# Kernel optimization log

Measured on AMD Instinct MI355X. Metric: run time of the kernel, lower is better.

## Reference

```python
import math
import jax, jax.numpy as jnp
import numpy as np

DIM = 2048
N_HEADS = 16
HEAD_DIM = DIM // N_HEADS
HID = 5632  # multiple_of*ceil(int(2*(4*dim)/3)/multiple_of)
EPS = 1e-5
B, S = 2, 2048


def setup_inputs() -> dict:
    key = jax.random.key(0)
    ks = jax.random.split(key, 12)
    sd = 0.02
    return {
        "x": jax.random.normal(ks[0], (B, S, DIM), jnp.float32),
        "mask": jnp.zeros((1, 1, S, S), jnp.float32),
        "attn_bias": jax.random.normal(ks[1], (1, N_HEADS, S, S), jnp.float32) * 0.1,
        "wq": jax.random.normal(ks[2], (DIM, DIM), jnp.float32) * sd,
        "wk": jax.random.normal(ks[3], (DIM, DIM), jnp.float32) * sd,
        "wv": jax.random.normal(ks[4], (DIM, DIM), jnp.float32) * sd,
        "wo": jax.random.normal(ks[5], (DIM, DIM), jnp.float32) * sd,
        "w1": jax.random.normal(ks[6], (HID, DIM), jnp.float32) * sd,
        "w2": jax.random.normal(ks[7], (DIM, HID), jnp.float32) * sd,
        "w3": jax.random.normal(ks[8], (HID, DIM), jnp.float32) * sd,
        "attn_norm_w": jnp.ones((DIM,), jnp.float32),
        "ffn_norm_w": jnp.ones((DIM,), jnp.float32),
    }


def rmsnorm(x, w):
    x32 = x.astype(jnp.float32)
    y = x32 * jax.lax.rsqrt(jnp.mean(x32 * x32, axis=-1, keepdims=True) + EPS)
    return y.astype(x.dtype) * w


def reference(x, mask, attn_bias, wq, wk, wv, wo, w1, w2, w3, attn_norm_w, ffn_norm_w):
    b, s, _ = x.shape
    # --- attention ---
    h = rmsnorm(x, attn_norm_w)
    q = (h @ wq.T).reshape(b, s, N_HEADS, HEAD_DIM)
    k = (h @ wk.T).reshape(b, s, N_HEADS, HEAD_DIM)
    v = (h @ wv.T).reshape(b, s, N_HEADS, HEAD_DIM)
    scores = jnp.einsum("bqhd,bkhd->bhqk", q, k) / math.sqrt(HEAD_DIM)
    scores = scores + attn_bias + mask
    probs = jax.nn.softmax(scores.astype(jnp.float32), axis=-1).astype(q.dtype)
    out = jnp.einsum("bhqk,bkhd->bqhd", probs, v).reshape(b, s, DIM)
    h1 = x + out @ wo.T
    # --- SwiGLU FFN ---
    f = rmsnorm(h1, ffn_norm_w)
    ff = (jax.nn.silu(f @ w1.T) * (f @ w3.T)) @ w2.T
    return h1 + ff
```

## Files before the change

### kernel.cpp

```cpp
#include <hip/hip_runtime.h>
#include <stdint.h>

typedef uint16_t u16;
typedef __attribute__((ext_vector_type(8))) short s16x8;
typedef __attribute__((ext_vector_type(4))) float f32x4;

typedef const __attribute__((address_space(1))) void* gptr_t;
typedef __attribute__((address_space(3))) void* lptr_t;

__device__ __forceinline__ float bf2f(u16 u) { return __uint_as_float(((unsigned)u) << 16); }
__device__ __forceinline__ u16 f2bf(float f) {
    unsigned u = __float_as_uint(f);
    u += 0x7fffu + ((u >> 16) & 1u);
    return (u16)(u >> 16);
}
__device__ __forceinline__ void gld_lds16(const void* g, void* l) {
    __builtin_amdgcn_global_load_lds((gptr_t)g, (lptr_t)l, 16, 0, 0);
}

__global__ __launch_bounds__(256) void cvt_f32_bf16(const float* __restrict__ src,
                                                    u16* __restrict__ dst, long n)
{
    const long i = ((long)blockIdx.x * 256 + threadIdx.x) * 8;
    if (i >= n) return;
    float4 a = *(const float4*)(src + i);
    float4 b = *(const float4*)(src + i + 4);
    u16 o8[8] = { f2bf(a.x), f2bf(a.y), f2bf(a.z), f2bf(a.w),
                  f2bf(b.x), f2bf(b.y), f2bf(b.z), f2bf(b.w) };
    *(uint4*)(dst + i) = *(const uint4*)o8;
}

__global__ __launch_bounds__(512, 2) void gemm256(
        const u16* __restrict__ A, const u16* __restrict__ B,
        u16* __restrict__ Cb, int M, int N, int K, int gx)
{
    __shared__ __align__(16) u16 As[2][256 * 64];
    __shared__ __align__(16) u16 Bs[2][256 * 64];

    const int tid  = threadIdx.x;
    const int wave = tid >> 6, lane = tid & 63;
    const int quad = lane >> 4, l16 = lane & 15;
    const int wmi = wave >> 2, wni = wave & 3;

    const int cpx = gridDim.x >> 3;
    const int wg  = ((int)blockIdx.x & 7) * cpx + ((int)blockIdx.x >> 3);
    const long m0 = (long)(wg / gx) * 256;
    const long n0 = (long)(wg % gx) * 256;

    f32x4 acc[8][4] = {};

    const u16* Ag = A + m0 * (long)K;
    const u16* Bg = B + n0 * (long)K;
    long soff[4];
    int  lbase[4];
#pragma unroll
    for (int i = 0; i < 4; i++) {
        const int c = i * 512 + tid;
        const int row = c >> 3, col8 = (c & 7) * 8;
        soff[i]  = (long)row * K + (col8 ^ ((row & 7) << 3));
        lbase[i] = (i * 512 + wave * 64) * 8;
    }

#pragma unroll
    for (int i = 0; i < 4; i++) {
        gld_lds16(Ag + soff[i], &As[0][lbase[i]]);
        gld_lds16(Bg + soff[i], &Bs[0][lbase[i]]);
    }
    __syncthreads();

    const int swz   = (l16 & 7) << 3;
    const int arow0 = wmi * 128 + l16;
    const int brow0 = wni * 64 + l16;

    int db = 0;
    for (int k0 = 0; k0 < K; k0 += 64) {
        const int  kn = k0 + 64;
        const bool pf = kn < K;
        s16x8 bfrag[4][2];
#pragma unroll
        for (int p = 0; p < 4; p++) {
            if (pf) {
                gld_lds16(Ag + soff[p] + kn, &As[db ^ 1][lbase[p]]);
                gld_lds16(Bg + soff[p] + kn, &Bs[db ^ 1][lbase[p]]);
            }
            if (p == 0) {
#pragma unroll
                for (int nt = 0; nt < 4; nt++)
#pragma unroll
                    for (int kk = 0; kk < 2; kk++)
                        bfrag[nt][kk] = *(const s16x8*)&Bs[db][(brow0 + nt * 16) * 64
                                            + ((kk * 32 + quad * 8) ^ swz)];
            }
            s16x8 af[2][2];
#pragma unroll
            for (int mtl = 0; mtl < 2; mtl++)
#pragma unroll
                for (int kk = 0; kk < 2; kk++)
                    af[mtl][kk] = *(const s16x8*)&As[db][(arow0 + (2 * p + mtl) * 16) * 64
                                        + ((kk * 32 + quad * 8) ^ swz)];
            __builtin_amdgcn_s_setprio(1);
#pragma unroll
            for (int mtl = 0; mtl < 2; mtl++)
#pragma unroll
                for (int nt = 0; nt < 4; nt++)
#pragma unroll
                    for (int kk = 0; kk < 2; kk++)
                        acc[2 * p + mtl][nt] = __builtin_amdgcn_mfma_f32_16x16x32_bf16(
                            af[mtl][kk], bfrag[nt][kk], acc[2 * p + mtl][nt], 0, 0, 0);
            __builtin_amdgcn_s_setprio(0);
        }
        __syncthreads();
        db ^= 1;
    }

#pragma unroll
    for (int mt = 0; mt < 8; mt++)
#pragma unroll
        for (int nt = 0; nt < 4; nt++) {
            const long col = n0 + wni * 64 + nt * 16 + l16;
#pragma unroll
            for (int r = 0; r < 4; r++) {
                const long row = m0 + wmi * 128 + mt * 16 + quad * 4 + r;
                Cb[row * (long)N + col] = f2bf(acc[mt][nt][r]);
            }
        }
}

__global__ __launch_bounds__(256) void gemm_bt(
        const u16* __restrict__ A, const u16* __restrict__ B,
        u16* __restrict__ Cb, float* __restrict__ Cf, const float* __restrict__ Rf,
        int M, int N, int K, int lda, int ep)
{
    __shared__ __align__(16) u16 As[128 * 32];
    __shared__ __align__(16) u16 Bs[128 * 32];

    const int tid  = threadIdx.x;
    const int wave = tid >> 6, lane = tid & 63;
    const int quad = lane >> 4, l16 = lane & 15;
    const long m0 = (long)blockIdx.y * 128, n0 = (long)blockIdx.x * 128;
    const int wm = (wave >> 1) * 64, wn = (wave & 1) * 64;

    f32x4 acc[4][4] = {};

    const int c0 = tid, c1 = tid + 256;
    const u16* Ag = A + m0 * (long)lda;
    const u16* Bg = B + n0 * (long)K;
    const long aA0 = (long)(c0 >> 2) * lda + (c0 & 3) * 8;
    const long aA1 = (long)(c1 >> 2) * lda + (c1 & 3) * 8;
    const long aB0 = (long)(c0 >> 2) * K + (c0 & 3) * 8;
    const long aB1 = (long)(c1 >> 2) * K + (c1 & 3) * 8;
    const int lb0 = (wave * 64) * 8;
    const int lb1 = (256 + wave * 64) * 8;

    for (int k0 = 0; k0 < K; k0 += 32) {
        __syncthreads();
        gld_lds16(Ag + aA0 + k0, &As[lb0]);
        gld_lds16(Ag + aA1 + k0, &As[lb1]);
        gld_lds16(Bg + aB0 + k0, &Bs[lb0]);
        gld_lds16(Bg + aB1 + k0, &Bs[lb1]);
        __syncthreads();

        s16x8 af[4], bfr[4];
#pragma unroll
        for (int t = 0; t < 4; t++) {
            af[t]  = *(const s16x8*)&As[(wm + t * 16 + l16) * 32 + quad * 8];
            bfr[t] = *(const s16x8*)&Bs[(wn + t * 16 + l16) * 32 + quad * 8];
        }
#pragma unroll
        for (int mt = 0; mt < 4; mt++)
#pragma unroll
            for (int nt = 0; nt < 4; nt++)
                acc[mt][nt] = __builtin_amdgcn_mfma_f32_16x16x32_bf16(
                    af[mt], bfr[nt], acc[mt][nt], 0, 0, 0);
    }

#pragma unroll
    for (int mt = 0; mt < 4; mt++)
#pragma unroll
        for (int nt = 0; nt < 4; nt++) {
            const long col = n0 + wn + nt * 16 + l16;
#pragma unroll
            for (int r = 0; r < 4; r++) {
                const long row = m0 + wm + mt * 16 + quad * 4 + r;
                const long idx = row * N + col;
                const float v = acc[mt][nt][r];
                if (ep == 0) Cb[idx] = f2bf(v);
                else         Cf[idx] = v + Rf[idx];
            }
        }
}

__global__ __launch_bounds__(256) void flash_attn(
        const u16* __restrict__ Q, const u16* __restrict__ Kp,
        const u16* __restrict__ V, int ld, const float* __restrict__ bias,
        const float* __restrict__ mask, u16* __restrict__ O)
{
    const int tid  = threadIdx.x;
    const int wave = tid >> 6, lane = tid & 63;
    const int quad = lane >> 4, l16 = lane & 15;
    const int q0 = blockIdx.x * 64, h = blockIdx.y, b = blockIdx.z;

    __shared__ __align__(16) u16 Ks[64 * 128];
    __shared__ __align__(16) u16 Vt[128 * 64];
    __shared__ __align__(16) u16 Ps[4][16 * 64];

    const long baseI = (long)b * 2048 * ld + (long)h * 128;
    const long baseO = (long)b * 2048 * 2048 + (long)h * 128;

    s16x8 qf[4];
    {
        const u16* qp = Q + baseI + (long)(q0 + wave * 16 + l16) * ld;
#pragma unroll
        for (int kk = 0; kk < 4; kk++)
            qf[kk] = *(const s16x8*)(qp + kk * 32 + quad * 8);
    }

    f32x4 oacc[8] = {};
    float m_i[4] = { -1e30f, -1e30f, -1e30f, -1e30f };
    float l_i[4] = { 0.f, 0.f, 0.f, 0.f };
    const float scale = 0.08838834764831845f;
    const int kswz = (l16 & 7) << 3;

    for (int k0 = 0; k0 < 2048; k0 += 64) {
        __syncthreads();
#pragma unroll
        for (int it = 0; it < 4; it++) {
            const int c = it * 256 + tid;
            const int row = c >> 4, col8 = (c & 15) * 8;
            const int src = col8 ^ ((row & 7) << 3);
            gld_lds16(Kp + baseI + (long)(k0 + row) * ld + src,
                      &Ks[(it * 256 + wave * 64) * 8]);
        }
#pragma unroll
        for (int it = 0; it < 4; it++) {
            const int c = it * 256 + tid;
            const int row = c >> 4, col8 = (c & 15) * 8;
            uint4 raw = *(const uint4*)(V + baseI + (long)(k0 + row) * ld + col8);
            const u16* e = (const u16*)&raw;
#pragma unroll
            for (int j = 0; j < 8; j++) {
                const int d = col8 + j;
                const int swzv = ((d & 7) ^ ((d >> 3) & 7)) << 3;
                Vt[d * 64 + (row ^ swzv)] = e[j];
            }
        }
        __syncthreads();

        float sv[4][4];
#pragma unroll
        for (int nt = 0; nt < 4; nt++) {
            f32x4 sa = { 0.f, 0.f, 0.f, 0.f };
#pragma unroll
            for (int kk = 0; kk < 4; kk++) {
                s16x8 kf = *(const s16x8*)&Ks[(nt * 16 + l16) * 128
                                              + ((kk * 32 + quad * 8) ^ kswz)];
                sa = __builtin_amdgcn_mfma_f32_16x16x32_bf16(qf[kk], kf, sa, 0, 0, 0);
            }
            const int kcol = k0 + nt * 16 + l16;
#pragma unroll
            for (int r = 0; r < 4; r++) {
                const int qrow = q0 + wave * 16 + quad * 4 + r;
                float val = sa[r] * scale;
                val += bias[((long)h * 2048 + qrow) * 2048 + kcol];
                val += mask[(long)qrow * 2048 + kcol];
                sv[nt][r] = val;
            }
        }

        float alpha[4];
#pragma unroll
        for (int r = 0; r < 4; r++) {
            float mx = fmaxf(fmaxf(sv[0][r], sv[1][r]), fmaxf(sv[2][r], sv[3][r]));
#pragma unroll
            for (int off = 1; off < 16; off <<= 1) mx = fmaxf(mx, __shfl_xor(mx, off));
            const float mnew = fmaxf(m_i[r], mx);
            alpha[r] = __expf(m_i[r] - mnew);
            m_i[r] = mnew;
            float rs = 0.f;
#pragma unroll
            for (int nt = 0; nt < 4; nt++) {
                const float pv = __expf(sv[nt][r] - mnew);
                sv[nt][r] = pv;
                rs += pv;
            }
#pragma unroll
            for (int off = 1; off < 16; off <<= 1) rs += __shfl_xor(rs, off);
            l_i[r] = l_i[r] * alpha[r] + rs;
        }

#pragma unroll
        for (int nt = 0; nt < 4; nt++)
#pragma unroll
            for (int r = 0; r < 4; r++) {
                const int prow = quad * 4 + r;
                Ps[wave][prow * 64 + ((nt * 16 + l16) ^ ((prow & 7) << 3))]
                    = f2bf(sv[nt][r]);
            }

#pragma unroll
        for (int dt = 0; dt < 8; dt++)
#pragma unroll
            for (int r = 0; r < 4; r++)
                oacc[dt][r] *= alpha[r];

#pragma unroll
        for (int kk2 = 0; kk2 < 2; kk2++) {
            s16x8 pf = *(const s16x8*)&Ps[wave][l16 * 64
                                               + ((kk2 * 32 + quad * 8) ^ kswz)];
#pragma unroll
            for (int dt = 0; dt < 8; dt++) {
                const int d = dt * 16 + l16;
                const int vswz = ((d & 7) ^ ((d >> 3) & 7)) << 3;
                s16x8 vf = *(const s16x8*)&Vt[d * 64
                                              + ((kk2 * 32 + quad * 8) ^ vswz)];
                oacc[dt] = __builtin_amdgcn_mfma_f32_16x16x32_bf16(pf, vf, oacc[dt], 0, 0, 0);
            }
        }
    }

#pragma unroll
    for (int dt = 0; dt < 8; dt++)
#pragma unroll
        for (int r = 0; r < 4; r++) {
            const int qrow = q0 + wave * 16 + quad * 4 + r;
            O[baseO + (long)qrow * 2048 + dt * 16 + l16] = f2bf(oacc[dt][r] / l_i[r]);
        }
}

__global__ __launch_bounds__(256) void rmsnorm_f32(
        const float* __restrict__ x, const float* __restrict__ w,
        u16* __restrict__ out)
{
    const int row = blockIdx.x, tid = threadIdx.x;
    const float* xr = x + (long)row * 2048;
    float4 f0 = *(const float4*)(xr + tid * 8);
    float4 f1 = *(const float4*)(xr + tid * 8 + 4);
    float v[8] = { f0.x, f0.y, f0.z, f0.w, f1.x, f1.y, f1.z, f1.w };
    float ss = 0.f;
#pragma unroll
    for (int j = 0; j < 8; j++) ss += v[j] * v[j];
#pragma unroll
    for (int off = 32; off > 0; off >>= 1) ss += __shfl_xor(ss, off);
    __shared__ float red[4];
    if ((tid & 63) == 0) red[tid >> 6] = ss;
    __syncthreads();
    const float tot = red[0] + red[1] + red[2] + red[3];
    const float sc = rsqrtf(tot * (1.0f / 2048.0f) + 1e-5f);
    float4 w0 = *(const float4*)(w + tid * 8);
    float4 w1v = *(const float4*)(w + tid * 8 + 4);
    const float wv[8] = { w0.x, w0.y, w0.z, w0.w, w1v.x, w1v.y, w1v.z, w1v.w };
    u16 o8[8];
#pragma unroll
    for (int j = 0; j < 8; j++) o8[j] = f2bf(v[j] * sc * wv[j]);
    *(uint4*)(out + (long)row * 2048 + tid * 8) = *(const uint4*)o8;
}

__global__ __launch_bounds__(704) void silu_mul_rows(u16* __restrict__ s13)
{
    const long rb = (long)blockIdx.x * 11264;
    const int col8 = threadIdx.x * 8;
    uint4 ra = *(const uint4*)(s13 + rb + col8);
    uint4 rbv = *(const uint4*)(s13 + rb + 5632 + col8);
    const u16* ea = (const u16*)&ra;
    const u16* eb = (const u16*)&rbv;
    u16 o8[8];
#pragma unroll
    for (int j = 0; j < 8; j++) {
        const float fa = bf2f(ea[j]);
        const float fb = bf2f(eb[j]);
        const float s = fa / (1.f + __expf(-fa));
        o8[j] = f2bf(s * fb);
    }
    *(uint4*)(s13 + rb + col8) = *(const uint4*)o8;
}

extern "C" void kernel_launch(void* const* d_in, const int* in_sizes, int n_in,
                              void* d_out, int out_size, void* d_ws, size_t ws_size,
                              hipStream_t stream)
{
    const float* x    = (const float*)d_in[0];
    const float* mask = (const float*)d_in[1];
    const float* bias = (const float*)d_in[2];
    const float* wq   = (const float*)d_in[3];
    const float* wk   = (const float*)d_in[4];
    const float* wv   = (const float*)d_in[5];
    const float* wo   = (const float*)d_in[6];
    const float* w1   = (const float*)d_in[7];
    const float* w2   = (const float*)d_in[8];
    const float* w3   = (const float*)d_in[9];
    const float* anw  = (const float*)d_in[10];
    const float* fnw  = (const float*)d_in[11];
    float* out = (float*)d_out;

    const long SZA = 2048L * 2048;
    const long SZF = 5632L * 2048;

    char* p = (char*)d_ws;
    u16* wqb = (u16*)p;  u16* wkb = wqb + SZA;  u16* wvb = wkb + SZA;
    u16* wob = wvb + SZA;
    u16* w1b = wob + SZA;  u16* w3b = w1b + SZF;  u16* w2b = w3b + SZF;
    p += (4 * SZA + 3 * SZF) * 2;
    const size_t SZ = (size_t)4096 * 2048 * 2;
    u16* h_buf  = (u16*)p;  p += SZ;
    u16* qkv    = (u16*)p;  p += (size_t)4096 * 6144 * 2;
    u16* s13    = (u16*)p;  p += (size_t)4096 * 11264 * 2;

    cvt_f32_bf16<<<2048, 256, 0, stream>>>(wq, wqb, SZA);
    cvt_f32_bf16<<<2048, 256, 0, stream>>>(wk, wkb, SZA);
    cvt_f32_bf16<<<2048, 256, 0, stream>>>(wv, wvb, SZA);
    cvt_f32_bf16<<<2048, 256, 0, stream>>>(wo, wob, SZA);
    cvt_f32_bf16<<<5632, 256, 0, stream>>>(w1, w1b, SZF);
    cvt_f32_bf16<<<5632, 256, 0, stream>>>(w3, w3b, SZF);
    cvt_f32_bf16<<<5632, 256, 0, stream>>>(w2, w2b, SZF);

    rmsnorm_f32<<<4096, 256, 0, stream>>>(x, anw, h_buf);
    gemm256<<<384, 512, 0, stream>>>(h_buf, wqb, qkv, 4096, 6144, 2048, 24);
    flash_attn<<<dim3(32, 16, 2), 256, 0, stream>>>(qkv, qkv + 2048, qkv + 4096,
                                                    6144, bias, mask, h_buf);
    gemm_bt<<<dim3(16, 32), 256, 0, stream>>>(h_buf, wob, nullptr, out, x,
                                              4096, 2048, 2048, 2048, 1);
    rmsnorm_f32<<<4096, 256, 0, stream>>>(out, fnw, h_buf);
    gemm256<<<704, 512, 0, stream>>>(h_buf, w1b, s13, 4096, 11264, 2048, 44);
    silu_mul_rows<<<4096, 704, 0, stream>>>(s13);
    gemm_bt<<<dim3(16, 32), 256, 0, stream>>>(s13, w2b, nullptr, out, out,
                                              4096, 2048, 5632, 11264, 1);
}
```

Before: 1.485 ms.

## Restructure bf16 GEMM main loop with explicit vmcnt-paced prefetch and phase barriers

Rewrites the K loop of the 256x256 bf16 GEMM so global-to-LDS loads for the next tile are issued in one batch and completion is tracked with explicit s_waitcnt vmcnt counters instead of a full __syncthreads. The B fragments are read once per step, and each of the four A/MFMA phases is fenced by raw s_barrier and sched_barrier to lock the instruction order and keep waves in lockstep. The intent is to overlap loads with MFMA work more predictably and cut full-sync stalls. In exchange it adds several workgroup barriers per K step, which may cost more than they save.

```diff
diff --git a/kernel.cpp b/kernel.cpp
--- a/kernel.cpp
+++ b/kernel.cpp
@@ -61,43 +61,55 @@
         lbase[i] = (i * 512 + wave * 64) * 8;
     }
 
-#pragma unroll
-    for (int i = 0; i < 4; i++) {
-        gld_lds16(Ag + soff[i], &As[0][lbase[i]]);
-        gld_lds16(Bg + soff[i], &Bs[0][lbase[i]]);
-    }
-    __syncthreads();
+    const int T = K >> 6;
+
+    auto issue = [&](int t, int slot) {
+#pragma unroll
+        for (int i = 0; i < 4; i++) {
+            gld_lds16(Ag + soff[i] + (long)t * 64, &As[slot][lbase[i]]);
+            gld_lds16(Bg + soff[i] + (long)t * 64, &Bs[slot][lbase[i]]);
+        }
+    };
+
+    issue(0, 0);
+    if (T > 1) issue(1, 1);
 
     const int swz   = (l16 & 7) << 3;
     const int arow0 = wmi * 128 + l16;
     const int brow0 = wni * 64 + l16;
 
-    int db = 0;
-    for (int k0 = 0; k0 < K; k0 += 64) {
-        const int  kn = k0 + 64;
-        const bool pf = kn < K;
+    for (int t = 0; t < T; ++t) {
+        const int slot = t & 1;
+        if (t + 1 < T) {
+            if (t >= 1) issue(t + 1, slot ^ 1);
+            asm volatile("s_waitcnt vmcnt(8)" ::: "memory");
+        } else {
+            asm volatile("s_waitcnt vmcnt(0)" ::: "memory");
+        }
+        __builtin_amdgcn_sched_barrier(0);
+        __builtin_amdgcn_s_barrier();
+        __builtin_amdgcn_sched_barrier(0);
+
         s16x8 bfrag[4][2];
 #pragma unroll
+        for (int nt = 0; nt < 4; nt++)
+#pragma unroll
+            for (int kk = 0; kk < 2; kk++)
+                bfrag[nt][kk] = *(const s16x8*)&Bs[slot][(brow0 + nt * 16) * 64
+                                    + ((kk * 32 + quad * 8) ^ swz)];
+
+#pragma unroll
         for (int p = 0; p < 4; p++) {
-            if (pf) {
-                gld_lds16(Ag + soff[p] + kn, &As[db ^ 1][lbase[p]]);
-                gld_lds16(Bg + soff[p] + kn, &Bs[db ^ 1][lbase[p]]);
-            }
-            if (p == 0) {
-#pragma unroll
-                for (int nt = 0; nt < 4; nt++)
-#pragma unroll
-                    for (int kk = 0; kk < 2; kk++)
-                        bfrag[nt][kk] = *(const s16x8*)&Bs[db][(brow0 + nt * 16) * 64
-                                            + ((kk * 32 + quad * 8) ^ swz)];
-            }
             s16x8 af[2][2];
 #pragma unroll
             for (int mtl = 0; mtl < 2; mtl++)
 #pragma unroll
                 for (int kk = 0; kk < 2; kk++)
-                    af[mtl][kk] = *(const s16x8*)&As[db][(arow0 + (2 * p + mtl) * 16) * 64
+                    af[mtl][kk] = *(const s16x8*)&As[slot][(arow0 + (2 * p + mtl) * 16) * 64
                                         + ((kk * 32 + quad * 8) ^ swz)];
+            __builtin_amdgcn_s_barrier();
+            asm volatile("s_waitcnt lgkmcnt(0)" ::: "memory");
+            __builtin_amdgcn_sched_barrier(0);
             __builtin_amdgcn_s_setprio(1);
 #pragma unroll
             for (int mtl = 0; mtl < 2; mtl++)
@@ -108,9 +120,8 @@
                         acc[2 * p + mtl][nt] = __builtin_amdgcn_mfma_f32_16x16x32_bf16(
                             af[mtl][kk], bfrag[nt][kk], acc[2 * p + mtl][nt], 0, 0, 0);
             __builtin_amdgcn_s_setprio(0);
-        }
-        __syncthreads();
-        db ^= 1;
+            __builtin_amdgcn_s_barrier();
+        }
     }
 
 #pragma unroll
```

Result: faster. 1.437 ms (-3.2%).
